# Kernel tuning notes

Measured on AMD Instinct MI355X. Metric: run time of the kernel, lower is better.

Reference implementation:

```python
import jax, jax.numpy as jnp
import numpy as np

T, B, N, GH, GW, ENC, H, D, TH = 16, 512, 8192, 3, 13, 128, 4, 32, 64
G = GH * GW          # 39 social grid cells
EMB = H * D          # 128 = n_head * att_out
SCALE = 1.0 / np.sqrt(ENC).astype(np.float32)
LN_EPS = 1e-5


def lstm(x, Wih, Whh, bih, bhh):
    # x: [T, Batch, in] -> hidden states [T, Batch, ENC]; torch gate order i,f,g,o
    n = x.shape[1]
    h0 = jnp.zeros((n, ENC), x.dtype)

    def step(carry, xt):
        h, c = carry
        g = xt @ Wih.T + bih + h @ Whh.T + bhh
        i, f, gg, o = jnp.split(g, 4, axis=-1)
        c = jax.nn.sigmoid(f) * c + jax.nn.sigmoid(i) * jnp.tanh(gg)
        h = jax.nn.sigmoid(o) * jnp.tanh(c)
        return (h, c), h

    _, hs = jax.lax.scan(step, (h0, h0), x)
    return hs


def glu(x, Wa, ba, Wg, bg):
    return (x @ Wa.T + ba) * jax.nn.sigmoid(x @ Wg.T + bg)


def layer_norm(x, g, b):
    m = jnp.mean(x, -1, keepdims=True)
    v = jnp.var(x, -1, keepdims=True)
    return (x - m) * jax.lax.rsqrt(v + LN_EPS) * g + b


def setup_inputs():
    key = jax.random.key(0)
    ks = jax.random.split(key, 40)

    def rn(i, sh, s=1.0):
        return jax.random.normal(ks[i], sh, jnp.float32) * s

    inp = {
        'hist': rn(0, (T, B, 2)), 'nbrs': rn(1, (T, N, 2)),
        'va': rn(2, (T, B, 2)), 'nbrsva': rn(3, (T, N, 2)),
        'lane': jnp.zeros((T, B, 1), jnp.float32),
        'nbrslane': jnp.zeros((T, N, 1), jnp.float32),
        'cls': rn(4, (T, B, 1)), 'nbrscls': rn(5, (T, N, 1)),
    }
    # boolean social-grid mask with exactly N true cells (cell-level, full enc dim)
    rng = np.random.default_rng(0)
    flat = np.zeros(B * G, bool)
    flat[rng.permutation(B * G)[:N]] = True
    inp['mask'] = jnp.asarray(np.broadcast_to(flat.reshape(B, GH, GW, 1), (B, GH, GW, ENC)))

    s = 0.05
    inp.update({
        'W1': rn(6, (TH, 5), s), 'b1': jnp.zeros((TH,), jnp.float32),
        'Wih': rn(7, (4 * ENC, TH), s), 'Whh': rn(8, (4 * ENC, ENC), s),
        'bih': jnp.zeros((4 * ENC,), jnp.float32), 'bhh': jnp.zeros((4 * ENC,), jnp.float32),
        'Wq': rn(9, (EMB, ENC), s), 'bq': jnp.zeros((EMB,), jnp.float32),
        'Wk': rn(10, (EMB, ENC), s), 'bk': jnp.zeros((EMB,), jnp.float32),
        'Wv': rn(11, (EMB, ENC), s), 'bv': jnp.zeros((EMB,), jnp.float32),
        'Wg1a': rn(12, (ENC, EMB), s), 'bg1a': jnp.zeros((ENC,), jnp.float32),
        'Wg1g': rn(13, (ENC, EMB), s), 'bg1g': jnp.zeros((ENC,), jnp.float32),
        'Wqt': rn(14, (EMB, ENC), s), 'bqt': jnp.zeros((EMB,), jnp.float32),
        'Wkt': rn(15, (EMB, ENC), s), 'bkt': jnp.zeros((EMB,), jnp.float32),
        'Wvt': rn(16, (EMB, ENC), s), 'bvt': jnp.zeros((EMB,), jnp.float32),
        'Wg2a': rn(17, (ENC, EMB), s), 'bg2a': jnp.zeros((ENC,), jnp.float32),
        'Wg2g': rn(18, (ENC, EMB), s), 'bg2g': jnp.zeros((ENC,), jnp.float32),
        'ln_g': jnp.ones((ENC,), jnp.float32), 'ln_b': jnp.zeros((ENC,), jnp.float32),
    })
    return inp


def reference(hist, nbrs, mask, va, nbrsva, lane, nbrslane, cls, nbrscls,
              W1, b1, Wih, Whh, bih, bhh, Wq, bq, Wk, bk, Wv, bv,
              Wg1a, bg1a, Wg1g, bg1g, Wqt, bqt, Wkt, bkt, Wvt, bvt,
              Wg2a, bg2a, Wg2g, bg2g, ln_g, ln_b):
    # f_length == 5 branch
    hist_in = jnp.concatenate((hist, cls, va), -1)        # [T,B,5]
    nbrs_in = jnp.concatenate((nbrs, nbrscls, nbrsva), -1)  # [T,N,5]

    hist_enc = jax.nn.elu(hist_in @ W1.T + b1)
    hist_h = lstm(hist_enc, Wih, Whh, bih, bhh)           # [T,B,ENC]
    hist_hidden = jnp.transpose(hist_h, (1, 0, 2))        # [B,T,ENC]

    nbrs_enc = jax.nn.elu(nbrs_in @ W1.T + b1)
    nbrs_h = lstm(nbrs_enc, Wih, Whh, bih, bhh)           # [T,N,ENC]

    # masked_scatter: fill true grid cells (row-major over B*G) with neighbor states
    cell = mask[:, :, :, 0].reshape(B * G)                # [B*G] bool
    idx = jnp.cumsum(cell.astype(jnp.int32)) - 1          # position among true cells
    gathered = nbrs_h[:, jnp.clip(idx, 0, N - 1), :]      # [T,B*G,ENC]
    soc = jnp.where(cell[None, :, None], gathered, 0.0).reshape(T, B, G, ENC)

    # spatial multi-head attention (each timestep attends over its own grid)
    q = (hist_hidden @ Wq.T + bq).reshape(B, T, H, D)
    k = (soc @ Wk.T + bk).reshape(T, B, G, H, D)
    v = (soc @ Wv.T + bv).reshape(T, B, G, H, D)
    a = jax.nn.softmax(jnp.einsum('bthd,tbghd->bthg', q, k) * SCALE, -1)
    spa = jnp.einsum('bthg,tbghd->bthd', a, v).reshape(B, T, EMB)
    spa = glu(spa, Wg1a, bg1a, Wg1g, bg1g)

    values = layer_norm(hist_hidden + spa, ln_g, ln_b)    # [B,T,ENC]

    # temporal multi-head attention over T
    qt = (values @ Wqt.T + bqt).reshape(B, T, H, D)
    kt = (values @ Wkt.T + bkt).reshape(B, T, H, D)
    vt = (values @ Wvt.T + bvt).reshape(B, T, H, D)
    at = jax.nn.softmax(jnp.einsum('bthd,bshd->bhts', qt, kt) * SCALE, -1)
    tmp = jnp.einsum('bhts,bshd->bthd', at, vt).reshape(B, T, EMB)
    tmp = glu(tmp, Wg2a, bg2a, Wg2g, bg2g)

    # use_spatial=True
    return layer_norm(hist_hidden + spa + tmp, ln_g, ln_b)
```

## Files before the change

kernel.cpp:

```cpp
#include <hip/hip_runtime.h>
#include <math.h>

#define T_ 16
#define B_ 512
#define N_ 8192
#define G_ 39
#define ENC_ 128
#define TH_ 64
#define MROWS 8704
#define GATE 512
#define KCAT 192
#define SCALE_ 0.08838834764831845f
#define LNEPS 1e-5f
#define NBLK 136

typedef short bf16x8 __attribute__((ext_vector_type(8)));
typedef float f32x4  __attribute__((ext_vector_type(4)));

__device__ __forceinline__ float sigm(float x){ return 1.0f/(1.0f+expf(-x)); }
__device__ __forceinline__ float rcpf(float x){ return __builtin_amdgcn_rcpf(x); }
__device__ __forceinline__ float sigm_f(float x){ return rcpf(1.0f + __expf(-x)); }
__device__ __forceinline__ float tanh_f(float x){ return 1.0f - 2.0f*rcpf(__expf(2.0f*x) + 1.0f); }
__device__ __forceinline__ unsigned short f2bf(float f){
  unsigned int u = __float_as_uint(f);
  unsigned int r = u + 0x7FFFu + ((u>>16)&1u);
  return (unsigned short)(r>>16);
}
__device__ __forceinline__ float bf2f(unsigned short h){
  return __uint_as_float(((unsigned int)h)<<16);
}

__global__ __launch_bounds__(256) void k_prep(
    const float* __restrict__ Wih, const float* __restrict__ Whh,
    const float* __restrict__ bih, const float* __restrict__ bhh,
    const float* __restrict__ Wk,  const float* __restrict__ bk,
    const float* __restrict__ Wv,  const float* __restrict__ bv,
    const float* __restrict__ Wq,
    const float* __restrict__ Wqt, const float* __restrict__ bqt,
    const float* __restrict__ Wkt, const float* __restrict__ bkt,
    const float* __restrict__ Wvt, const float* __restrict__ bvt,
    const float* __restrict__ Wg1a, const float* __restrict__ bg1a,
    const float* __restrict__ Wg1g, const float* __restrict__ bg1g,
    const float* __restrict__ Wg2a, const float* __restrict__ bg2a,
    const float* __restrict__ Wg2g, const float* __restrict__ bg2g,
    unsigned short* __restrict__ WcatB, float* __restrict__ biasg,
    unsigned short* __restrict__ WkvB,  float* __restrict__ bkv,
    unsigned short* __restrict__ WqB,
    unsigned short* __restrict__ WqktB, float* __restrict__ bqkt,
    unsigned short* __restrict__ Wg1B,  float* __restrict__ bg1,
    unsigned short* __restrict__ Wg2B,  float* __restrict__ bg2)
{
  int i = blockIdx.x*256 + threadIdx.x;
  if (i < GATE*KCAT) {
    int n = i / KCAT, k = i % KCAT;
    WcatB[i] = f2bf((k < TH_) ? Wih[n*TH_ + k] : Whh[n*ENC_ + (k - TH_)]);
  }
  if (i < GATE) biasg[i] = bih[i] + bhh[i];
  if (i < 2*ENC_*ENC_) {
    int n = i >> 7, k = i & 127;
    WkvB[i] = f2bf((n < ENC_) ? Wk[n*ENC_ + k] : Wv[(n-ENC_)*ENC_ + k]);
    Wg1B[i] = f2bf((n < ENC_) ? Wg1a[n*ENC_ + k] : Wg1g[(n-ENC_)*ENC_ + k]);
    Wg2B[i] = f2bf((n < ENC_) ? Wg2a[n*ENC_ + k] : Wg2g[(n-ENC_)*ENC_ + k]);
  }
  if (i < 2*ENC_) {
    bkv[i] = (i < ENC_) ? bk[i] : bv[i-ENC_];
    bg1[i] = (i < ENC_) ? bg1a[i] : bg1g[i-ENC_];
    bg2[i] = (i < ENC_) ? bg2a[i] : bg2g[i-ENC_];
  }
  if (i < ENC_*ENC_) WqB[i] = f2bf(Wq[i]);
  if (i < 3*ENC_*ENC_) {
    int n = i >> 7, k = i & 127;
    float w = (n < ENC_) ? Wqt[n*ENC_ + k] : (n < 2*ENC_) ? Wkt[(n-ENC_)*ENC_ + k]
                                                          : Wvt[(n-2*ENC_)*ENC_ + k];
    WqktB[i] = f2bf(w);
  }
  if (i < 3*ENC_) bqkt[i] = (i < ENC_) ? bqt[i] : (i < 2*ENC_) ? bkt[i-ENC_] : bvt[i-2*ENC_];
}

__device__ __forceinline__ int cellval(const unsigned char* m, long cell, int w) {
  long byte = cell * 128L * w;
  if (w == 1) return m[byte] != 0;
  if (w == 2) return *(const unsigned short*)(m + byte) != 0;
  if (w == 4) return *(const unsigned int*)(m + byte) != 0;
  return *(const unsigned long long*)(m + byte) != 0ULL;
}
__device__ __forceinline__ int cellconsist(const unsigned char* m, long cell, int w) {
  long byte = cell * 128L * w;
  if (w == 1) { unsigned char v = m[byte];
    for (int j = 1; j < 8; ++j) if (m[byte + j] != v) return 0; return 1; }
  if (w == 2) { unsigned short v = *(const unsigned short*)(m + byte);
    for (int j = 1; j < 8; ++j) if (*(const unsigned short*)(m + byte + 2L*j) != v) return 0; return 1; }
  if (w == 4) { unsigned int v = *(const unsigned int*)(m + byte);
    for (int j = 1; j < 8; ++j) if (*(const unsigned int*)(m + byte + 4L*j) != v) return 0; return 1; }
  unsigned long long v = *(const unsigned long long*)(m + byte);
  for (int j = 1; j < 8; ++j) if (*(const unsigned long long*)(m + byte + 8L*j) != v) return 0; return 1;
}

__global__ void k_detect(const unsigned char* __restrict__ mask, int* __restrict__ wsel)
{
  __shared__ int bad;
  int tid = threadIdx.x;
  int chosen = 0;
  for (int w = 1; w <= 8 && !chosen; w <<= 1) {
    if (tid == 0) bad = 0;
    __syncthreads();
    int ok = 1;
    for (int c = tid; c < 512; c += 256) ok &= cellconsist(mask, c, w);
    if (!ok) bad = 1;
    __syncthreads();
    if (!bad) chosen = w;
    __syncthreads();
  }
  if (tid == 0) *wsel = chosen ? chosen : 1;
}

__global__ void k_count(const unsigned char* __restrict__ mask,
                        const int* __restrict__ wsel, int* __restrict__ bcnt)
{
  __shared__ int sc[256];
  int tid = threadIdx.x;
  long cell = (long)blockIdx.x*256 + tid;
  sc[tid] = cellval(mask, cell, *wsel);
  __syncthreads();
  for (int off = 128; off; off >>= 1) {
    if (tid < off) sc[tid] += sc[tid + off];
    __syncthreads();
  }
  if (tid == 0) bcnt[blockIdx.x] = sc[0];
}

__global__ void k_fill(const unsigned char* __restrict__ mask,
                       const int* __restrict__ wsel, const int* __restrict__ bcnt,
                       int* __restrict__ nidx)
{
  __shared__ int sc[256];
  int tid = threadIdx.x, blk = blockIdx.x;
  long cell = (long)blk*256 + tid;
  int on = cellval(mask, cell, *wsel);
  sc[tid] = on;
  __syncthreads();
  for (int off = 1; off < 256; off <<= 1) {
    int v = (tid >= off) ? sc[tid - off] : 0;
    __syncthreads();
    sc[tid] += v;
    __syncthreads();
  }
  int base = 0;
  for (int i = 0; i < blk; ++i) base += bcnt[i];
  nidx[cell] = on ? (base + sc[tid] - 1) : -1;
}

struct AP {
  const float *hist, *cls, *va, *nbrs, *nbrscls, *nbrsva;
  const float *W1, *b1;
  const unsigned short *Wcat, *Wkv, *Wq;
  const float *biasg, *bkv, *bq;
  float *hh;
  float *qbuf;
  unsigned short *knvB;
  unsigned short *Hsp;
  float *csp;
  int c0, tch;
};

__global__ __launch_bounds__(512, 2) void k_lstm(AP p)
{
  __shared__ unsigned short Hl[2*64*128];
  __shared__ unsigned short Xl[64*64];
  __shared__ float finl[16][64][5];

  const int tid = threadIdx.x;
  const int w = tid >> 6, l = tid & 63;
  const int lr = l & 15, lk = (l >> 4) * 8, lq = (l >> 4) * 4;
  const int bi = blockIdx.x, bm = bi * 64;
  const bool ish = (bi < 8);

  bf16x8 wg[4][6];
  #pragma unroll
  for (int g = 0; g < 4; ++g)
    #pragma unroll
    for (int ks = 0; ks < 6; ++ks)
      wg[g][ks] = *(const bf16x8*)(p.Wcat + (long)(g*128 + w*16 + lr)*KCAT + ks*32 + lk);

  const int ch = w*16 + lr;
  const float bgi = p.biasg[ch], bgf = p.biasg[128+ch],
              bgg = p.biasg[256+ch], bgo = p.biasg[384+ch];

  const float w1c0 = p.W1[l*5+0], w1c1 = p.W1[l*5+1], w1c2 = p.W1[l*5+2],
              w1c3 = p.W1[l*5+3], w1c4 = p.W1[l*5+4], b1c = p.b1[l];

  for (int idx = tid; idx < p.tch*320; idx += 512) {
    int t4 = idx / 320, rem = idx - t4*320;
    int row = rem / 5, f = rem - row*5;
    long r = ish ? ((long)(p.c0 + t4)*B_ + bm + row) : ((long)(p.c0 + t4)*N_ + (bm - B_) + row);
    const float* ph = ish ? p.hist : p.nbrs;
    const float* pc = ish ? p.cls  : p.nbrscls;
    const float* pv = ish ? p.va   : p.nbrsva;
    finl[t4][row][f] = (f < 2) ? ph[r*2 + f] : (f == 2) ? pc[r] : pv[r*2 + (f-3)];
  }

  float creg[4][4];
  if (p.c0 == 0) {
    for (int i = tid; i < 64*128; i += 512) Hl[i] = 0;
    #pragma unroll
    for (int mi = 0; mi < 4; ++mi)
      #pragma unroll
      for (int q = 0; q < 4; ++q) creg[mi][q] = 0.0f;
  } else {
    for (int i = tid; i < 64*128; i += 512) Hl[i] = p.Hsp[(long)bm*128 + i];
    #pragma unroll
    for (int mi = 0; mi < 4; ++mi)
      #pragma unroll
      for (int q = 0; q < 4; ++q) creg[mi][q] = p.csp[((long)bi*512 + tid)*16 + mi*4 + q];
  }
  __syncthreads();

  int cur = 0;
  for (int tl = 0; tl < p.tch; ++tl) {
    int t = p.c0 + tl;
    {
      #pragma unroll
      for (int j = 0; j < 8; ++j) {
        int row = w*8 + j;
        float s = b1c + finl[tl][row][0]*w1c0 + finl[tl][row][1]*w1c1
                      + finl[tl][row][2]*w1c2 + finl[tl][row][3]*w1c3
                      + finl[tl][row][4]*w1c4;
        s = (s > 0.0f) ? s : expm1f(s);
        Xl[row*64 + (l ^ ((row & 7) << 3))] = f2bf(s);
      }
    }
    __syncthreads();
    f32x4 acc[4][4] = {};
    #pragma unroll
    for (int ks = 0; ks < 2; ++ks) {
      bf16x8 a[4];
      #pragma unroll
      for (int mi = 0; mi < 4; ++mi) {
        int row = mi*16 + lr;
        int col = (ks*32 + lk) ^ ((row & 7) << 3);
        a[mi] = *(const bf16x8*)(Xl + row*64 + col);
      }
      #pragma unroll
      for (int g = 0; g < 4; ++g)
        #pragma unroll
        for (int mi = 0; mi < 4; ++mi)
          acc[g][mi] = __builtin_amdgcn_mfma_f32_16x16x32_bf16(a[mi], wg[g][ks], acc[g][mi], 0, 0, 0);
    }
    #pragma unroll
    for (int ks = 0; ks < 4; ++ks) {
      bf16x8 a[4];
      #pragma unroll
      for (int mi = 0; mi < 4; ++mi) {
        int row = mi*16 + lr;
        int col = (ks*32 + lk) ^ ((row & 7) << 3);
        a[mi] = *(const bf16x8*)(Hl + cur*8192 + row*128 + col);
      }
      #pragma unroll
      for (int g = 0; g < 4; ++g)
        #pragma unroll
        for (int mi = 0; mi < 4; ++mi)
          acc[g][mi] = __builtin_amdgcn_mfma_f32_16x16x32_bf16(a[mi], wg[g][2+ks], acc[g][mi], 0, 0, 0);
    }
    int nxt = cur ^ 1;
    #pragma unroll
    for (int mi = 0; mi < 4; ++mi)
      #pragma unroll
      for (int q = 0; q < 4; ++q) {
        int row = mi*16 + lq + q;
        float gi = acc[0][mi][q] + bgi;
        float gf = acc[1][mi][q] + bgf;
        float gg = acc[2][mi][q] + bgg;
        float go = acc[3][mi][q] + bgo;
        float cc = sigm_f(gf)*creg[mi][q] + sigm_f(gi)*tanh_f(gg);
        creg[mi][q] = cc;
        float hv = sigm_f(go)*tanh_f(cc);
        Hl[nxt*8192 + row*128 + (ch ^ ((row & 7) << 3))] = f2bf(hv);
        if (ish) p.hh[((long)(bm + row)*T_ + t)*128 + ch] = hv;
      }
    __syncthreads();
    cur = nxt;
    if (!ish) {
      f32x4 a2[4][2] = {};
      #pragma unroll
      for (int ks = 0; ks < 4; ++ks) {
        bf16x8 a[4];
        #pragma unroll
        for (int mi = 0; mi < 4; ++mi) {
          int row = mi*16 + lr;
          int col = (ks*32 + lk) ^ ((row & 7) << 3);
          a[mi] = *(const bf16x8*)(Hl + cur*8192 + row*128 + col);
        }
        #pragma unroll
        for (int ni = 0; ni < 2; ++ni) {
          bf16x8 b = *(const bf16x8*)(p.Wkv + (long)(w*32 + ni*16 + lr)*128 + ks*32 + lk);
          #pragma unroll
          for (int mi = 0; mi < 4; ++mi)
            a2[mi][ni] = __builtin_amdgcn_mfma_f32_16x16x32_bf16(a[mi], b, a2[mi][ni], 0, 0, 0);
        }
      }
      long nr = bm - B_;
      #pragma unroll
      for (int mi = 0; mi < 4; ++mi)
        #pragma unroll
        for (int ni = 0; ni < 2; ++ni) {
          int c2 = w*32 + ni*16 + lr;
          float bb = p.bkv[c2];
          #pragma unroll
          for (int q = 0; q < 4; ++q)
            p.knvB[((long)tl*N_ + nr + mi*16 + lq + q)*256 + c2] = f2bf(a2[mi][ni][q] + bb);
        }
    } else {
      f32x4 a2[4] = {};
      #pragma unroll
      for (int ks = 0; ks < 4; ++ks) {
        bf16x8 a[4];
        #pragma unroll
        for (int mi = 0; mi < 4; ++mi) {
          int row = mi*16 + lr;
          int col = (ks*32 + lk) ^ ((row & 7) << 3);
          a[mi] = *(const bf16x8*)(Hl + cur*8192 + row*128 + col);
        }
        bf16x8 b = *(const bf16x8*)(p.Wq + (long)(w*16 + lr)*128 + ks*32 + lk);
        #pragma unroll
        for (int mi = 0; mi < 4; ++mi)
          a2[mi] = __builtin_amdgcn_mfma_f32_16x16x32_bf16(a[mi], b, a2[mi], 0, 0, 0);
      }
      float bb = p.bq[ch];
      #pragma unroll
      for (int mi = 0; mi < 4; ++mi)
        #pragma unroll
        for (int q = 0; q < 4; ++q)
          p.qbuf[((long)t*B_ + bm + mi*16 + lq + q)*128 + ch] = a2[mi][q] + bb;
    }
    __syncthreads();
  }
  for (int i = tid; i < 64*128; i += 512) p.Hsp[(long)bm*128 + i] = Hl[cur*8192 + i];
  #pragma unroll
  for (int mi = 0; mi < 4; ++mi)
    #pragma unroll
    for (int q = 0; q < 4; ++q)
      p.csp[((long)bi*512 + tid)*16 + mi*4 + q] = creg[mi][q];
}

__global__ __launch_bounds__(256) void k_attn_sp(
    int c0, int ltch,
    const float* __restrict__ qbuf, const unsigned short* __restrict__ knvB,
    const float* __restrict__ bk, const float* __restrict__ bv,
    const int* __restrict__ nidx, unsigned short* __restrict__ spaB)
{
  int tid = threadIdx.x;
  int w = tid >> 6, l = tid & 63;
  __shared__ int sn[4][G_];
  __shared__ float aw[4][4][40];
  int gwid = blockIdx.x*4 + w;
  int b = gwid >> ltch;
  int tl = gwid & ((1 << ltch) - 1);
  int t = c0 + tl;
  if (l < G_) sn[w][l] = nidx[b*G_ + l];
  __syncthreads();
  float qA = qbuf[((long)t*B_ + b)*128 + l];
  float qB = qbuf[((long)t*B_ + b)*128 + 64 + l];
  for (int g = 0; g < G_; ++g) {
    int ni = sn[w][g];
    const unsigned short* kr = knvB + ((long)tl*N_ + ni)*256;
    float kA = (ni >= 0) ? bf2f(kr[l])      : bk[l];
    float kB = (ni >= 0) ? bf2f(kr[64 + l]) : bk[64 + l];
    float pA = qA*kA, pB = qB*kB;
    pA += __shfl_xor(pA, 16); pA += __shfl_xor(pA, 8); pA += __shfl_xor(pA, 4);
    pA += __shfl_xor(pA, 2);  pA += __shfl_xor(pA, 1);
    pB += __shfl_xor(pB, 16); pB += __shfl_xor(pB, 8); pB += __shfl_xor(pB, 4);
    pB += __shfl_xor(pB, 2);  pB += __shfl_xor(pB, 1);
    if ((l & 31) == 0) {
      int hb = l >> 5;
      aw[w][hb][g]     = pA * SCALE_;
      aw[w][2+hb][g]   = pB * SCALE_;
    }
  }
  __syncthreads();
  int hA = l >> 5, hB = 2 + (l >> 5);
  float mxA = -1e30f, mxB = -1e30f;
  for (int g = 0; g < G_; ++g) {
    mxA = fmaxf(mxA, aw[w][hA][g]);
    mxB = fmaxf(mxB, aw[w][hB][g]);
  }
  float sA = 0.f, sB = 0.f, oA = 0.f, oB = 0.f;
  for (int g = 0; g < G_; ++g) {
    int ni = sn[w][g];
    const unsigned short* vr = knvB + ((long)tl*N_ + ni)*256 + 128;
    float vA = (ni >= 0) ? bf2f(vr[l])      : bv[l];
    float vB = (ni >= 0) ? bf2f(vr[64 + l]) : bv[64 + l];
    float eA = expf(aw[w][hA][g] - mxA);
    float eB = expf(aw[w][hB][g] - mxB);
    sA += eA; sB += eB; oA += eA*vA; oB += eB*vB;
  }
  spaB[((long)b*T_ + t)*128 + l]      = f2bf(oA / sA);
  spaB[((long)b*T_ + t)*128 + 64 + l] = f2bf(oB / sB);
}

__global__ __launch_bounds__(256) void k_gemm_bf16(
    const unsigned short* __restrict__ A, int lda,
    const unsigned short* __restrict__ W, int ldw,
    const float* __restrict__ bias,
    float* __restrict__ C, int ldc, int K)
{
  int tid = threadIdx.x;
  int w = tid >> 6, l = tid & 63;
  int lr = l & 15, lk = (l >> 4) * 8, lq = (l >> 4) * 4;
  int bm = blockIdx.x * 64;
  int bn = blockIdx.y * 128 + w * 32;
  f32x4 acc[4][2] = {};
  for (int k0 = 0; k0 < K; k0 += 32) {
    bf16x8 a[4], b[2];
    #pragma unroll
    for (int mi = 0; mi < 4; ++mi)
      a[mi] = *(const bf16x8*)(A + (long)(bm + mi*16 + lr)*lda + k0 + lk);
    #pragma unroll
    for (int ni = 0; ni < 2; ++ni)
      b[ni] = *(const bf16x8*)(W + (long)(bn + ni*16 + lr)*ldw + k0 + lk);
    #pragma unroll
    for (int mi = 0; mi < 4; ++mi)
      #pragma unroll
      for (int ni = 0; ni < 2; ++ni)
        acc[mi][ni] = __builtin_amdgcn_mfma_f32_16x16x32_bf16(a[mi], b[ni], acc[mi][ni], 0, 0, 0);
  }
  #pragma unroll
  for (int mi = 0; mi < 4; ++mi)
    #pragma unroll
    for (int ni = 0; ni < 2; ++ni) {
      int col = bn + ni*16 + lr;
      float bb = bias[col];
      #pragma unroll
      for (int q = 0; q < 4; ++q)
        C[(long)(bm + mi*16 + lq + q)*ldc + col] = acc[mi][ni][q] + bb;
    }
}

__global__ __launch_bounds__(256) void k_gemm_bf16o(
    const unsigned short* __restrict__ A, int lda,
    const unsigned short* __restrict__ W, int ldw,
    const float* __restrict__ bias,
    unsigned short* __restrict__ C, int ldc, int K)
{
  int tid = threadIdx.x;
  int w = tid >> 6, l = tid & 63;
  int lr = l & 15, lk = (l >> 4) * 8, lq = (l >> 4) * 4;
  int bm = blockIdx.x * 64;
  int bn = blockIdx.y * 128 + w * 32;
  f32x4 acc[4][2] = {};
  for (int k0 = 0; k0 < K; k0 += 32) {
    bf16x8 a[4], b[2];
    #pragma unroll
    for (int mi = 0; mi < 4; ++mi)
      a[mi] = *(const bf16x8*)(A + (long)(bm + mi*16 + lr)*lda + k0 + lk);
    #pragma unroll
    for (int ni = 0; ni < 2; ++ni)
      b[ni] = *(const bf16x8*)(W + (long)(bn + ni*16 + lr)*ldw + k0 + lk);
    #pragma unroll
    for (int mi = 0; mi < 4; ++mi)
      #pragma unroll
      for (int ni = 0; ni < 2; ++ni)
        acc[mi][ni] = __builtin_amdgcn_mfma_f32_16x16x32_bf16(a[mi], b[ni], acc[mi][ni], 0, 0, 0);
  }
  #pragma unroll
  for (int mi = 0; mi < 4; ++mi)
    #pragma unroll
    for (int ni = 0; ni < 2; ++ni) {
      int col = bn + ni*16 + lr;
      float bb = bias[col];
      #pragma unroll
      for (int q = 0; q < 4; ++q)
        C[(long)(bm + mi*16 + lq + q)*ldc + col] = f2bf(acc[mi][ni][q] + bb);
    }
}

__global__ __launch_bounds__(256) void k_glu_addln(
    const float* __restrict__ t12, const float* __restrict__ res,
    const float* __restrict__ lg, const float* __restrict__ lb,
    float* __restrict__ sum_out, unsigned short* __restrict__ ln_bf16,
    float* __restrict__ ln_f32)
{
  int gtid = blockIdx.x*256 + threadIdx.x;
  int r = gtid >> 6;
  int l = threadIdx.x & 63;
  if (r >= B_*T_) return;
  long b4 = (long)r*256, b2 = (long)r*128;
  float xA = res[b2 + l]      + t12[b4 + l]      * sigm(t12[b4 + 128 + l]);
  float xB = res[b2 + 64 + l] + t12[b4 + 64 + l] * sigm(t12[b4 + 192 + l]);
  if (sum_out) { sum_out[b2 + l] = xA; sum_out[b2 + 64 + l] = xB; }
  float s = xA + xB, s2 = xA*xA + xB*xB;
  #pragma unroll
  for (int off = 32; off; off >>= 1) { s += __shfl_xor(s, off); s2 += __shfl_xor(s2, off); }
  float mean = s * (1.0f/128.0f);
  float var  = s2 * (1.0f/128.0f) - mean*mean;
  float inv  = rsqrtf(var + LNEPS);
  float oA = (xA - mean)*inv*lg[l]      + lb[l];
  float oB = (xB - mean)*inv*lg[64 + l] + lb[64 + l];
  if (ln_bf16) { ln_bf16[b2 + l] = f2bf(oA); ln_bf16[b2 + 64 + l] = f2bf(oB); }
  if (ln_f32)  { ln_f32[b2 + l] = oA;        ln_f32[b2 + 64 + l] = oB; }
}

__global__ __launch_bounds__(128) void k_attn_t(
    const unsigned short* __restrict__ qkt, unsigned short* __restrict__ out)
{
  int b = blockIdx.x, tid = threadIdx.x;
  __shared__ float sq[16][128], sk[16][128], sv[16][128];
  __shared__ float sc[16][4][16];
  for (int i = tid; i < T_*ENC_; i += 128) {
    int tt = i >> 7, j = i & 127;
    long a = ((long)b*T_ + tt)*384;
    sq[tt][j] = bf2f(qkt[a + j]);
    sk[tt][j] = bf2f(qkt[a + 128 + j]);
    sv[tt][j] = bf2f(qkt[a + 256 + j]);
  }
  __syncthreads();
  for (int e = tid; e < 1024; e += 128) {
    int t = e >> 6, s = (e >> 2) & 15, h2 = e & 3;
    float pp = 0.0f;
    #pragma unroll
    for (int d2 = 0; d2 < 32; ++d2) pp += sq[t][h2*32 + d2] * sk[s][h2*32 + d2];
    sc[t][h2][s] = pp * SCALE_;
  }
  __syncthreads();
  if (tid < 64) {
    int t = tid >> 2, h2 = tid & 3;
    float mx = -1e30f;
    for (int s = 0; s < 16; ++s) mx = fmaxf(mx, sc[t][h2][s]);
    float sum = 0.0f;
    for (int s = 0; s < 16; ++s) { float e2 = expf(sc[t][h2][s] - mx); sc[t][h2][s] = e2; sum += e2; }
    float inv = 1.0f / sum;
    for (int s = 0; s < 16; ++s) sc[t][h2][s] *= inv;
  }
  __syncthreads();
  int h2 = tid >> 5, d2 = tid & 31;
  for (int t = 0; t < 16; ++t) {
    float acc = 0.0f;
    for (int s = 0; s < 16; ++s) acc += sc[t][h2][s] * sv[s][h2*32 + d2];
    out[((long)b*T_ + t)*128 + tid] = f2bf(acc);
  }
}

extern "C" void kernel_launch(void* const* d_in, const int* in_sizes, int n_in,
                              void* d_out, int out_size, void* d_ws, size_t ws_size,
                              hipStream_t stream)
{
  const float* hist    = (const float*)d_in[0];
  const float* nbrs    = (const float*)d_in[1];
  const float* va      = (const float*)d_in[2];
  const float* nbrsva  = (const float*)d_in[3];
  const float* cls     = (const float*)d_in[6];
  const float* nbrscls = (const float*)d_in[7];
  const unsigned char* mask = (const unsigned char*)d_in[8];
  const float* W1  = (const float*)d_in[9];
  const float* b1  = (const float*)d_in[10];
  const float* Wih = (const float*)d_in[11];
  const float* Whh = (const float*)d_in[12];
  const float* bih = (const float*)d_in[13];
  const float* bhh = (const float*)d_in[14];
  const float* Wq  = (const float*)d_in[15];
  const float* bq  = (const float*)d_in[16];
  const float* Wk  = (const float*)d_in[17];
  const float* bk  = (const float*)d_in[18];
  const float* Wv  = (const float*)d_in[19];
  const float* bv  = (const float*)d_in[20];
  const float* Wg1a = (const float*)d_in[21];
  const float* bg1a = (const float*)d_in[22];
  const float* Wg1g = (const float*)d_in[23];
  const float* bg1g = (const float*)d_in[24];
  const float* Wqt = (const float*)d_in[25];
  const float* bqt = (const float*)d_in[26];
  const float* Wkt = (const float*)d_in[27];
  const float* bkt = (const float*)d_in[28];
  const float* Wvt = (const float*)d_in[29];
  const float* bvt = (const float*)d_in[30];
  const float* Wg2a = (const float*)d_in[31];
  const float* bg2a = (const float*)d_in[32];
  const float* Wg2g = (const float*)d_in[33];
  const float* bg2g = (const float*)d_in[34];
  const float* ln_g = (const float*)d_in[35];
  const float* ln_b = (const float*)d_in[36];

  size_t fixed = 0;
  {
    size_t items[] = {
      (size_t)GATE*KCAT*2, (size_t)GATE*4, (size_t)2*ENC_*ENC_*2, (size_t)2*ENC_*4,
      (size_t)ENC_*ENC_*2, (size_t)3*ENC_*ENC_*2, (size_t)3*ENC_*4,
      (size_t)2*ENC_*ENC_*2, (size_t)2*ENC_*4, (size_t)2*ENC_*ENC_*2, (size_t)2*ENC_*4,
      (size_t)B_*T_*ENC_*4,
      (size_t)T_*B_*ENC_*4,
      (size_t)MROWS*ENC_*2,
      (size_t)NBLK*512*16*4,
      (size_t)B_*T_*ENC_*2,
      (size_t)B_*T_*2*ENC_*4,
      (size_t)B_*T_*ENC_*4,
      (size_t)B_*T_*ENC_*2,
      (size_t)B_*T_*3*ENC_*2,
      (size_t)B_*T_*ENC_*2,
      (size_t)B_*G_*4, (size_t)78*4, (size_t)4
    };
    for (size_t v : items) fixed += (v + 255) & ~(size_t)255;
  }
  int tch = 16, ltch = 4;
  while (tch > 4 && fixed + ((size_t)tch*N_*256*2 + 255) > ws_size) { tch >>= 1; ltch--; }

  char* base = (char*)d_ws;
  size_t off = 0;
  auto alloc = [&](size_t bytes) { char* r = base + off; off = (off + bytes + 255) & ~(size_t)255; return r; };
  unsigned short* WcatB = (unsigned short*)alloc(GATE*KCAT*2);
  float*          biasg = (float*)alloc(GATE*4);
  unsigned short* WkvB  = (unsigned short*)alloc(2*ENC_*ENC_*2);
  float*          bkv   = (float*)alloc(2*ENC_*4);
  unsigned short* WqB   = (unsigned short*)alloc(ENC_*ENC_*2);
  unsigned short* WqktB = (unsigned short*)alloc(3*ENC_*ENC_*2);
  float*          bqkt  = (float*)alloc(3*ENC_*4);
  unsigned short* Wg1B  = (unsigned short*)alloc(2*ENC_*ENC_*2);
  float*          bg1   = (float*)alloc(2*ENC_*4);
  unsigned short* Wg2B  = (unsigned short*)alloc(2*ENC_*ENC_*2);
  float*          bg2   = (float*)alloc(2*ENC_*4);
  float*          hh    = (float*)alloc((size_t)B_*T_*ENC_*4);
  float*          qbuf  = (float*)alloc((size_t)T_*B_*ENC_*4);
  unsigned short* Hsp   = (unsigned short*)alloc((size_t)MROWS*ENC_*2);
  float*          csp   = (float*)alloc((size_t)NBLK*512*16*4);
  unsigned short* spaB  = (unsigned short*)alloc((size_t)B_*T_*ENC_*2);
  float*          t12   = (float*)alloc((size_t)B_*T_*2*ENC_*4);
  float*          S1    = (float*)alloc((size_t)B_*T_*ENC_*4);
  unsigned short* valsB = (unsigned short*)alloc((size_t)B_*T_*ENC_*2);
  unsigned short* qktB  = (unsigned short*)alloc((size_t)B_*T_*3*ENC_*2);
  unsigned short* atoB  = (unsigned short*)alloc((size_t)B_*T_*ENC_*2);
  int*            nidx  = (int*)alloc((size_t)B_*G_*4);
  int*            bcnt  = (int*)alloc(78*4);
  int*            wsel  = (int*)alloc(4);
  unsigned short* knvB  = (unsigned short*)alloc((size_t)tch*N_*256*2);

  k_prep<<<384, 256, 0, stream>>>(
      Wih, Whh, bih, bhh, Wk, bk, Wv, bv, Wq,
      Wqt, bqt, Wkt, bkt, Wvt, bvt,
      Wg1a, bg1a, Wg1g, bg1g, Wg2a, bg2a, Wg2g, bg2g,
      WcatB, biasg, WkvB, bkv, WqB, WqktB, bqkt, Wg1B, bg1, Wg2B, bg2);
  k_detect<<<1, 256, 0, stream>>>(mask, wsel);
  k_count<<<78, 256, 0, stream>>>(mask, wsel, bcnt);
  k_fill<<<78, 256, 0, stream>>>(mask, wsel, bcnt, nidx);

  AP ap;
  ap.hist = hist; ap.cls = cls; ap.va = va;
  ap.nbrs = nbrs; ap.nbrscls = nbrscls; ap.nbrsva = nbrsva;
  ap.W1 = W1; ap.b1 = b1;
  ap.Wcat = WcatB; ap.Wkv = WkvB; ap.Wq = WqB;
  ap.biasg = biasg; ap.bkv = bkv; ap.bq = bq;
  ap.hh = hh; ap.qbuf = qbuf; ap.knvB = knvB; ap.Hsp = Hsp; ap.csp = csp;
  ap.tch = tch;
  for (int c0 = 0; c0 < T_; c0 += tch) {
    ap.c0 = c0;
    k_lstm<<<NBLK, 512, 0, stream>>>(ap);
    k_attn_sp<<<(B_*tch)/4, 256, 0, stream>>>(c0, ltch, qbuf, knvB, bk, bv, nidx, spaB);
  }

  k_gemm_bf16<<<dim3((B_*T_)/64, 2), 256, 0, stream>>>(spaB, 128, Wg1B, 128, bg1, t12, 256, 128);
  k_glu_addln<<<(B_*T_*64)/256, 256, 0, stream>>>(t12, hh, ln_g, ln_b, S1, valsB, nullptr);
  k_gemm_bf16o<<<dim3((B_*T_)/64, 3), 256, 0, stream>>>(valsB, 128, WqktB, 128, bqkt, qktB, 384, 128);
  k_attn_t<<<B_, 128, 0, stream>>>(qktB, atoB);
  k_gemm_bf16<<<dim3((B_*T_)/64, 2), 256, 0, stream>>>(atoB, 128, Wg2B, 128, bg2, t12, 256, 128);
  k_glu_addln<<<(B_*T_*64)/256, 256, 0, stream>>>(t12, S1, ln_g, ln_b, nullptr, nullptr, (float*)d_out);
}
```

Measured before the change: 310.6 us.

## Halve LSTM block row tile to double grid and precompute input projections

The LSTM kernel now handles 32 rows per block instead of 64 and launches 272 blocks instead of 136, spreading the serial recurrence across more CUs. The input-layer ELU features for every timestep in the chunk are computed once up front into shared memory, which removes a per-step shared-memory write and barrier. The input-part gate weights are no longer held in registers; they are reloaded from global memory each step, which lowers register pressure but adds global or cache traffic. The minimum time-chunk size drops from 4 to 2, and the cell-state spill buffer layout is adjusted to match.

Result: slower. 341.3 us (+9.9%).

```diff
diff --git a/kernel.cpp b/kernel.cpp
--- a/kernel.cpp
+++ b/kernel.cpp
@@ -12,7 +12,7 @@
 #define KCAT 192
 #define SCALE_ 0.08838834764831845f
 #define LNEPS 1e-5f
-#define NBLK 136
+#define NBLK2 272
 
 typedef short bf16x8 __attribute__((ext_vector_type(8)));
 typedef float f32x4  __attribute__((ext_vector_type(4)));
@@ -165,105 +165,98 @@
 
 __global__ __launch_bounds__(512, 2) void k_lstm(AP p)
 {
-  __shared__ unsigned short Hl[2*64*128];
-  __shared__ unsigned short Xl[64*64];
-  __shared__ float finl[16][64][5];
+  __shared__ unsigned short Hl[2*32*128];
+  __shared__ unsigned short Xall[16*32*64];
 
   const int tid = threadIdx.x;
   const int w = tid >> 6, l = tid & 63;
   const int lr = l & 15, lk = (l >> 4) * 8, lq = (l >> 4) * 4;
-  const int bi = blockIdx.x, bm = bi * 64;
-  const bool ish = (bi < 8);
-
-  bf16x8 wg[4][6];
+  const int bi = blockIdx.x, bm = bi * 32;
+  const bool ish = (bi < 16);
+
+  bf16x8 wgh[4][4];
   #pragma unroll
   for (int g = 0; g < 4; ++g)
     #pragma unroll
-    for (int ks = 0; ks < 6; ++ks)
-      wg[g][ks] = *(const bf16x8*)(p.Wcat + (long)(g*128 + w*16 + lr)*KCAT + ks*32 + lk);
+    for (int ks = 0; ks < 4; ++ks)
+      wgh[g][ks] = *(const bf16x8*)(p.Wcat + (long)(g*128 + w*16 + lr)*KCAT + 64 + ks*32 + lk);
 
   const int ch = w*16 + lr;
   const float bgi = p.biasg[ch], bgf = p.biasg[128+ch],
               bgg = p.biasg[256+ch], bgo = p.biasg[384+ch];
 
-  const float w1c0 = p.W1[l*5+0], w1c1 = p.W1[l*5+1], w1c2 = p.W1[l*5+2],
-              w1c3 = p.W1[l*5+3], w1c4 = p.W1[l*5+4], b1c = p.b1[l];
-
-  for (int idx = tid; idx < p.tch*320; idx += 512) {
-    int t4 = idx / 320, rem = idx - t4*320;
-    int row = rem / 5, f = rem - row*5;
-    long r = ish ? ((long)(p.c0 + t4)*B_ + bm + row) : ((long)(p.c0 + t4)*N_ + (bm - B_) + row);
+  {
+    const float w1c0 = p.W1[l*5+0], w1c1 = p.W1[l*5+1], w1c2 = p.W1[l*5+2],
+                w1c3 = p.W1[l*5+3], w1c4 = p.W1[l*5+4], b1c = p.b1[l];
     const float* ph = ish ? p.hist : p.nbrs;
     const float* pc = ish ? p.cls  : p.nbrscls;
     const float* pv = ish ? p.va   : p.nbrsva;
-    finl[t4][row][f] = (f < 2) ? ph[r*2 + f] : (f == 2) ? pc[r] : pv[r*2 + (f-3)];
-  }
-
-  float creg[4][4];
+    for (int e = w; e < p.tch*32; e += 8) {
+      int t4 = e >> 5, row = e & 31;
+      long r = ish ? ((long)(p.c0 + t4)*B_ + bm + row)
+                   : ((long)(p.c0 + t4)*N_ + (bm - B_) + row);
+      float i0 = ph[r*2], i1 = ph[r*2+1], i2 = pc[r], i3 = pv[r*2], i4 = pv[r*2+1];
+      float s = b1c + i0*w1c0 + i1*w1c1 + i2*w1c2 + i3*w1c3 + i4*w1c4;
+      s = (s > 0.0f) ? s : expm1f(s);
+      Xall[(t4*32 + row)*64 + (l ^ ((row & 7) << 3))] = f2bf(s);
+    }
+  }
+
+  float creg[2][4];
   if (p.c0 == 0) {
-    for (int i = tid; i < 64*128; i += 512) Hl[i] = 0;
-    #pragma unroll
-    for (int mi = 0; mi < 4; ++mi)
+    for (int i = tid; i < 32*128; i += 512) Hl[i] = 0;
+    #pragma unroll
+    for (int mi = 0; mi < 2; ++mi)
       #pragma unroll
       for (int q = 0; q < 4; ++q) creg[mi][q] = 0.0f;
   } else {
-    for (int i = tid; i < 64*128; i += 512) Hl[i] = p.Hsp[(long)bm*128 + i];
-    #pragma unroll
-    for (int mi = 0; mi < 4; ++mi)
-      #pragma unroll
-      for (int q = 0; q < 4; ++q) creg[mi][q] = p.csp[((long)bi*512 + tid)*16 + mi*4 + q];
+    for (int i = tid; i < 32*128; i += 512) Hl[i] = p.Hsp[(long)bm*128 + i];
+    #pragma unroll
+    for (int mi = 0; mi < 2; ++mi)
+      #pragma unroll
+      for (int q = 0; q < 4; ++q) creg[mi][q] = p.csp[((long)bi*512 + tid)*8 + mi*4 + q];
   }
   __syncthreads();
 
   int cur = 0;
   for (int tl = 0; tl < p.tch; ++tl) {
     int t = p.c0 + tl;
-    {
-      #pragma unroll
-      for (int j = 0; j < 8; ++j) {
-        int row = w*8 + j;
-        float s = b1c + finl[tl][row][0]*w1c0 + finl[tl][row][1]*w1c1
-                      + finl[tl][row][2]*w1c2 + finl[tl][row][3]*w1c3
-                      + finl[tl][row][4]*w1c4;
-        s = (s > 0.0f) ? s : expm1f(s);
-        Xl[row*64 + (l ^ ((row & 7) << 3))] = f2bf(s);
+    f32x4 acc[4][2] = {};
+    #pragma unroll
+    for (int ks = 0; ks < 2; ++ks) {
+      bf16x8 a[2];
+      #pragma unroll
+      for (int mi = 0; mi < 2; ++mi) {
+        int row = mi*16 + lr;
+        int col = (ks*32 + lk) ^ ((row & 7) << 3);
+        a[mi] = *(const bf16x8*)(Xall + (tl*32 + row)*64 + col);
+      }
+      #pragma unroll
+      for (int g = 0; g < 4; ++g) {
+        bf16x8 b = *(const bf16x8*)(p.Wcat + (long)(g*128 + w*16 + lr)*KCAT + ks*32 + lk);
+        #pragma unroll
+        for (int mi = 0; mi < 2; ++mi)
+          acc[g][mi] = __builtin_amdgcn_mfma_f32_16x16x32_bf16(a[mi], b, acc[g][mi], 0, 0, 0);
       }
     }
-    __syncthreads();
-    f32x4 acc[4][4] = {};
-    #pragma unroll
-    for (int ks = 0; ks < 2; ++ks) {
-      bf16x8 a[4];
-      #pragma unroll
-      for (int mi = 0; mi < 4; ++mi) {
+    #pragma unroll
+    for (int ks = 0; ks < 4; ++ks) {
+      bf16x8 a[2];
+      #pragma unroll
+      for (int mi = 0; mi < 2; ++mi) {
         int row = mi*16 + lr;
         int col = (ks*32 + lk) ^ ((row & 7) << 3);
-        a[mi] = *(const bf16x8*)(Xl + row*64 + col);
+        a[mi] = *(const bf16x8*)(Hl + cur*4096 + row*128 + col);
       }
       #pragma unroll
       for (int g = 0; g < 4; ++g)
         #pragma unroll
-        for (int mi = 0; mi < 4; ++mi)
-          acc[g][mi] = __builtin_amdgcn_mfma_f32_16x16x32_bf16(a[mi], wg[g][ks], acc[g][mi], 0, 0, 0);
-    }
-    #pragma unroll
-    for (int ks = 0; ks < 4; ++ks) {
-      bf16x8 a[4];
-      #pragma unroll
-      for (int mi = 0; mi < 4; ++mi) {
-        int row = mi*16 + lr;
-        int col = (ks*32 + lk) ^ ((row & 7) << 3);
-        a[mi] = *(const bf16x8*)(Hl + cur*8192 + row*128 + col);
-      }
-      #pragma unroll
-      for (int g = 0; g < 4; ++g)
-        #pragma unroll
-        for (int mi = 0; mi < 4; ++mi)
-          acc[g][mi] = __builtin_amdgcn_mfma_f32_16x16x32_bf16(a[mi], wg[g][2+ks], acc[g][mi], 0, 0, 0);
+        for (int mi = 0; mi < 2; ++mi)
+          acc[g][mi] = __builtin_amdgcn_mfma_f32_16x16x32_bf16(a[mi], wgh[g][ks], acc[g][mi], 0, 0, 0);
     }
     int nxt = cur ^ 1;
     #pragma unroll
-    for (int mi = 0; mi < 4; ++mi)
+    for (int mi = 0; mi < 2; ++mi)
       #pragma unroll
       for (int q = 0; q < 4; ++q) {
         int row = mi*16 + lq + q;
@@ -274,33 +267,33 @@
         float cc = sigm_f(gf)*creg[mi][q] + sigm_f(gi)*tanh_f(gg);
         creg[mi][q] = cc;
         float hv = sigm_f(go)*tanh_f(cc);
-        Hl[nxt*8192 + row*128 + (ch ^ ((row & 7) << 3))] = f2bf(hv);
+        Hl[nxt*4096 + row*128 + (ch ^ ((row & 7) << 3))] = f2bf(hv);
         if (ish) p.hh[((long)(bm + row)*T_ + t)*128 + ch] = hv;
       }
     __syncthreads();
     cur = nxt;
     if (!ish) {
-      f32x4 a2[4][2] = {};
+      f32x4 a2[2][2] = {};
       #pragma unroll
       for (int ks = 0; ks < 4; ++ks) {
-        bf16x8 a[4];
-        #pragma unroll
-        for (int mi = 0; mi < 4; ++mi) {
+        bf16x8 a[2];
+        #pragma unroll
+        for (int mi = 0; mi < 2; ++mi) {
           int row = mi*16 + lr;
           int col = (ks*32 + lk) ^ ((row & 7) << 3);
-          a[mi] = *(const bf16x8*)(Hl + cur*8192 + row*128 + col);
+          a[mi] = *(const bf16x8*)(Hl + cur*4096 + row*128 + col);
         }
         #pragma unroll
         for (int ni = 0; ni < 2; ++ni) {
           bf16x8 b = *(const bf16x8*)(p.Wkv + (long)(w*32 + ni*16 + lr)*128 + ks*32 + lk);
           #pragma unroll
-          for (int mi = 0; mi < 4; ++mi)
+          for (int mi = 0; mi < 2; ++mi)
             a2[mi][ni] = __builtin_amdgcn_mfma_f32_16x16x32_bf16(a[mi], b, a2[mi][ni], 0, 0, 0);
         }
       }
       long nr = bm - B_;
       #pragma unroll
-      for (int mi = 0; mi < 4; ++mi)
+      for (int mi = 0; mi < 2; ++mi)
         #pragma unroll
         for (int ni = 0; ni < 2; ++ni) {
           int c2 = w*32 + ni*16 + lr;
@@ -310,36 +303,36 @@
             p.knvB[((long)tl*N_ + nr + mi*16 + lq + q)*256 + c2] = f2bf(a2[mi][ni][q] + bb);
         }
     } else {
-      f32x4 a2[4] = {};
+      f32x4 a2[2] = {};
       #pragma unroll
       for (int ks = 0; ks < 4; ++ks) {
-        bf16x8 a[4];
-        #pragma unroll
-        for (int mi = 0; mi < 4; ++mi) {
+        bf16x8 a[2];
+        #pragma unroll
+        for (int mi = 0; mi < 2; ++mi) {
           int row = mi*16 + lr;
           int col = (ks*32 + lk) ^ ((row & 7) << 3);
-          a[mi] = *(const bf16x8*)(Hl + cur*8192 + row*128 + col);
+          a[mi] = *(const bf16x8*)(Hl + cur*4096 + row*128 + col);
         }
         bf16x8 b = *(const bf16x8*)(p.Wq + (long)(w*16 + lr)*128 + ks*32 + lk);
         #pragma unroll
-        for (int mi = 0; mi < 4; ++mi)
+        for (int mi = 0; mi < 2; ++mi)
           a2[mi] = __builtin_amdgcn_mfma_f32_16x16x32_bf16(a[mi], b, a2[mi], 0, 0, 0);
       }
       float bb = p.bq[ch];
       #pragma unroll
-      for (int mi = 0; mi < 4; ++mi)
+      for (int mi = 0; mi < 2; ++mi)
         #pragma unroll
         for (int q = 0; q < 4; ++q)
           p.qbuf[((long)t*B_ + bm + mi*16 + lq + q)*128 + ch] = a2[mi][q] + bb;
     }
     __syncthreads();
   }
-  for (int i = tid; i < 64*128; i += 512) p.Hsp[(long)bm*128 + i] = Hl[cur*8192 + i];
+  for (int i = tid; i < 32*128; i += 512) p.Hsp[(long)bm*128 + i] = Hl[cur*4096 + i];
   #pragma unroll
-  for (int mi = 0; mi < 4; ++mi)
+  for (int mi = 0; mi < 2; ++mi)
     #pragma unroll
     for (int q = 0; q < 4; ++q)
-      p.csp[((long)bi*512 + tid)*16 + mi*4 + q] = creg[mi][q];
+      p.csp[((long)bi*512 + tid)*8 + mi*4 + q] = creg[mi][q];
 }
 
 __global__ __launch_bounds__(256) void k_attn_sp(
@@ -588,7 +581,7 @@
       (size_t)B_*T_*ENC_*4,
       (size_t)T_*B_*ENC_*4,
       (size_t)MROWS*ENC_*2,
-      (size_t)NBLK*512*16*4,
+      (size_t)NBLK2*512*8*4,
       (size_t)B_*T_*ENC_*2,
       (size_t)B_*T_*2*ENC_*4,
       (size_t)B_*T_*ENC_*4,
@@ -600,7 +593,7 @@
     for (size_t v : items) fixed += (v + 255) & ~(size_t)255;
   }
   int tch = 16, ltch = 4;
-  while (tch > 4 && fixed + ((size_t)tch*N_*256*2 + 255) > ws_size) { tch >>= 1; ltch--; }
+  while (tch > 2 && fixed + ((size_t)tch*N_*256*2 + 255) > ws_size) { tch >>= 1; ltch--; }
 
   char* base = (char*)d_ws;
   size_t off = 0;
@@ -619,7 +612,7 @@
   float*          hh    = (float*)alloc((size_t)B_*T_*ENC_*4);
   float*          qbuf  = (float*)alloc((size_t)T_*B_*ENC_*4);
   unsigned short* Hsp   = (unsigned short*)alloc((size_t)MROWS*ENC_*2);
-  float*          csp   = (float*)alloc((size_t)NBLK*512*16*4);
+  float*          csp   = (float*)alloc((size_t)NBLK2*512*8*4);
   unsigned short* spaB  = (unsigned short*)alloc((size_t)B_*T_*ENC_*2);
   float*          t12   = (float*)alloc((size_t)B_*T_*2*ENC_*4);
   float*          S1    = (float*)alloc((size_t)B_*T_*ENC_*4);
@@ -650,7 +643,7 @@
   ap.tch = tch;
   for (int c0 = 0; c0 < T_; c0 += tch) {
     ap.c0 = c0;
-    k_lstm<<<NBLK, 512, 0, stream>>>(ap);
+    k_lstm<<<NBLK2, 512, 0, stream>>>(ap);
     k_attn_sp<<<(B_*tch)/4, 256, 0, stream>>>(c0, ltch, qbuf, knvB, bk, bv, nidx, spaB);
   }
 
```
